# Kernel optimization log

Measured on AMD Instinct MI355X. Metric: run time of the kernel, lower is better.

The kernel has to match this reference:

```python
import jax, jax.numpy as jnp
import numpy as np

NUM_FRAMES = 64
H, W = 2048, 2048
MAX_DEPTH = 12


def setup_inputs() -> dict:
    key = jax.random.key(0)
    k1, k2, k3 = jax.random.split(key, 3)
    frame_colors = jax.random.uniform(k1, (NUM_FRAMES, 3), dtype=jnp.float32)
    frame_selection = jax.random.uniform(k2, (NUM_FRAMES, 2, NUM_FRAMES), dtype=jnp.float32)
    split_ratios = jax.random.uniform(k3, (NUM_FRAMES,), dtype=jnp.float32)
    return {
        "frame_colors": frame_colors,
        "frame_selection": frame_selection,
        "split_ratios": split_ratios,
    }


def reference(frame_colors, frame_selection, split_ratios):
    """Vectorized per-pixel descent of the bounded fractal recursion.

    Instead of recursive slice-assignments with host-synced argmax/.item(),
    each pixel tracks (frame idx, region origin, region size) and descends
    MAX_DEPTH levels via gathers. Equivalent math to render_frame(0,...).
    """
    # Per-frame child indices (argmax over the selection logits).
    left_child = jnp.argmax(frame_selection[:, 0, :], axis=-1).astype(jnp.int32)   # [F]
    right_child = jnp.argmax(frame_selection[:, 1, :], axis=-1).astype(jnp.int32)  # [F]

    yy, xx = jnp.meshgrid(jnp.arange(H, dtype=jnp.int32),
                          jnp.arange(W, dtype=jnp.int32), indexing="ij")  # [H,W]

    idx = jnp.zeros((H, W), jnp.int32)   # current frame index per pixel
    y0 = jnp.zeros((H, W), jnp.int32)    # region origin
    x0 = jnp.zeros((H, W), jnp.int32)
    h = jnp.full((H, W), H, jnp.int32)   # region size
    w = jnp.full((H, W), W, jnp.int32)
    done = jnp.zeros((H, W), bool)

    for _ in range(MAX_DEPTH):
        leaf = (w < 2) | (h < 2)            # base case: region too small
        act = (~done) & (~leaf)             # pixels that descend this level
        done = done | leaf

        ratio = split_ratios[idx]                       # [H,W]
        is_vert = (idx % 2) == 1                        # split_directions = i % 2
        # left_width = max(1, int(width * ratio)); analogous top_height
        lw = jnp.maximum(1, jnp.floor(w.astype(jnp.float32) * ratio).astype(jnp.int32))
        th = jnp.maximum(1, jnp.floor(h.astype(jnp.float32) * ratio).astype(jnp.int32))

        go_left = jnp.where(is_vert, (xx - x0) < lw, (yy - y0) < th)
        child = jnp.where(go_left, left_child[idx], right_child[idx])

        nx0 = jnp.where(is_vert & (~go_left), x0 + lw, x0)
        nw = jnp.where(is_vert, jnp.where(go_left, lw, w - lw), w)
        ny0 = jnp.where((~is_vert) & (~go_left), y0 + th, y0)
        nh = jnp.where(~is_vert, jnp.where(go_left, th, h - th), h)

        idx = jnp.where(act, child, idx)
        x0 = jnp.where(act, nx0, x0)
        w = jnp.where(act, nw, w)
        y0 = jnp.where(act, ny0, y0)
        h = jnp.where(act, nh, h)

    # Fill each pixel with its leaf frame's background color -> [3, H, W]
    out = frame_colors[idx]                 # [H, W, 3]
    return jnp.transpose(out, (2, 0, 1))
```

## Files before the change

### kernel.cpp

```cpp
#include <hip/hip_runtime.h>

#define HH_DIM 2048
#define WW_DIM 2048
#define NF 64
#define MAX_DEPTH 12

__global__ void child_argmax_kernel(const float* __restrict__ sel,
                                    int* __restrict__ child) {
    int r = threadIdx.x;
    if (r < 2 * NF) {
        const float* row = sel + r * NF;
        float best = row[0];
        int bi = 0;
        #pragma unroll
        for (int j = 1; j < NF; ++j) {
            float v = row[j];
            if (v > best) { best = v; bi = j; }
        }
        child[r] = bi;
    }
}

__global__ __launch_bounds__(256)
void render_kernel(const float* __restrict__ colors,
                   const float* __restrict__ ratios,
                   const int* __restrict__ child,
                   float* __restrict__ out) {
    __shared__ float s_ratio[NF];
    __shared__ int   s_child[2 * NF];
    __shared__ float s_col[3 * NF];

    int t = threadIdx.x;
    if (t < NF)      s_ratio[t] = ratios[t];
    if (t < 2 * NF)  s_child[t] = child[t];
    if (t < 3 * NF)  s_col[t]   = colors[t];
    __syncthreads();

    int gid = blockIdx.x * 256 + t;
    int y  = gid >> 9;
    int xb = (gid & 511) << 2;

    float c0[4], c1[4], c2[4];

    #pragma unroll
    for (int p = 0; p < 4; ++p) {
        int x = xb + p;
        int idx = 0;
        int x0 = 0, y0 = 0, w = WW_DIM, h = HH_DIM;
        for (int d = 0; d < MAX_DEPTH; ++d) {
            if (w < 2 || h < 2) break;
            float ratio = s_ratio[idx];
            int ni;
            if (idx & 1) {
                int lw = (int)floorf((float)w * ratio);
                lw = lw < 1 ? 1 : lw;
                bool left = (x - x0) < lw;
                ni = left ? s_child[2 * idx] : s_child[2 * idx + 1];
                if (left) { w = lw; }
                else      { x0 += lw; w -= lw; }
            } else {
                int th = (int)floorf((float)h * ratio);
                th = th < 1 ? 1 : th;
                bool left = (y - y0) < th;
                ni = left ? s_child[2 * idx] : s_child[2 * idx + 1];
                if (left) { h = th; }
                else      { y0 += th; h -= th; }
            }
            idx = ni;
        }
        c0[p] = s_col[idx * 3 + 0];
        c1[p] = s_col[idx * 3 + 1];
        c2[p] = s_col[idx * 3 + 2];
    }

    int base = y * WW_DIM + xb;
    const int plane = HH_DIM * WW_DIM;
    *(float4*)(out + base)             = make_float4(c0[0], c0[1], c0[2], c0[3]);
    *(float4*)(out + plane + base)     = make_float4(c1[0], c1[1], c1[2], c1[3]);
    *(float4*)(out + 2 * plane + base) = make_float4(c2[0], c2[1], c2[2], c2[3]);
}

extern "C" void kernel_launch(void* const* d_in, const int* in_sizes, int n_in,
                              void* d_out, int out_size, void* d_ws, size_t ws_size,
                              hipStream_t stream) {
    const float* frame_colors    = (const float*)d_in[0];
    const float* frame_selection = (const float*)d_in[1];
    const float* split_ratios    = (const float*)d_in[2];
    float* out = (float*)d_out;
    int* child = (int*)d_ws;

    child_argmax_kernel<<<1, 128, 0, stream>>>(frame_selection, child);

    render_kernel<<<4096, 256, 0, stream>>>(frame_colors, split_ratios, child, out);
}
```

Measured before the change: 96.69 us.

## Fuse argmax into render kernel and reuse descent across leaf-region pixel runs

The separate argmax launch is removed: every block recomputes the child indices from the selection logits in shared memory. Each thread now owns a 16-pixel strip of one row and runs the tree descent once per leaf region rather than once per pixel, filling every pixel up to the region's right edge. Leaf indices are packed as bytes into shared memory, then the block writes all three colour planes with coalesced float4 stores through a planar colour table. This cuts the per-pixel descent work and one launch, at the cost of redundant per-block argmax, an extra barrier and divergent while-loops across a wavefront.

Result: slower. 98.79 us (+2.2%).

```diff
diff --git a/kernel.cpp b/kernel.cpp
--- a/kernel.cpp
+++ b/kernel.cpp
@@ -1,83 +1,118 @@
 #include <hip/hip_runtime.h>
 
-#define HH_DIM 2048
-#define WW_DIM 2048
+#define HH 2048
+#define WW 2048
 #define NF 64
-#define MAX_DEPTH 12
+#define MAXD 12
+#define ROWS_PER_BLOCK 2
+#define STRIP 16
+#define PXB (ROWS_PER_BLOCK * WW)
 
-__global__ void child_argmax_kernel(const float* __restrict__ sel,
-                                    int* __restrict__ child) {
-    int r = threadIdx.x;
-    if (r < 2 * NF) {
-        const float* row = sel + r * NF;
-        float best = row[0];
+__global__ __launch_bounds__(256)
+void fractal_kernel(const float* __restrict__ colors,
+                    const float* __restrict__ sel,
+                    const float* __restrict__ ratios,
+                    float* __restrict__ out) {
+    __shared__ int2  s_node[NF];
+    __shared__ float s_colp[3 * NF];
+    __shared__ int   s_amax[2 * NF];
+    __shared__ unsigned char s_idx[PXB];
+
+    int t = threadIdx.x;
+
+    if (t < 2 * NF) {
+        const float4* row = (const float4*)(sel + t * NF);
+        float4 v0 = row[0];
+        float best = v0.x;
         int bi = 0;
         #pragma unroll
-        for (int j = 1; j < NF; ++j) {
-            float v = row[j];
-            if (v > best) { best = v; bi = j; }
+        for (int j = 0; j < NF / 4; ++j) {
+            float4 v = row[j];
+            if (v.x > best) { best = v.x; bi = 4 * j + 0; }
+            if (v.y > best) { best = v.y; bi = 4 * j + 1; }
+            if (v.z > best) { best = v.z; bi = 4 * j + 2; }
+            if (v.w > best) { best = v.w; bi = 4 * j + 3; }
         }
-        child[r] = bi;
+        s_amax[t] = bi;
     }
-}
-
-__global__ __launch_bounds__(256)
-void render_kernel(const float* __restrict__ colors,
-                   const float* __restrict__ ratios,
-                   const int* __restrict__ child,
-                   float* __restrict__ out) {
-    __shared__ float s_ratio[NF];
-    __shared__ int   s_child[2 * NF];
-    __shared__ float s_col[3 * NF];
-
-    int t = threadIdx.x;
-    if (t < NF)      s_ratio[t] = ratios[t];
-    if (t < 2 * NF)  s_child[t] = child[t];
-    if (t < 3 * NF)  s_col[t]   = colors[t];
+    if (t < NF) {
+        s_node[t].x = __float_as_int(ratios[t]);
+    }
+    if (t < 3 * NF) {
+        int f = t / 3, c = t - 3 * f;
+        s_colp[c * NF + f] = colors[t];
+    }
+    __syncthreads();
+    if (t < NF) {
+        s_node[t].y = s_amax[2 * t] | (s_amax[2 * t + 1] << 16);
+    }
     __syncthreads();
 
-    int gid = blockIdx.x * 256 + t;
-    int y  = gid >> 9;
-    int xb = (gid & 511) << 2;
+    int r  = t >> 7;
+    int c  = t & 127;
+    int y  = blockIdx.x * ROWS_PER_BLOCK + r;
+    int xb = c * STRIP;
+    int xend = xb + STRIP;
+    int x = xb;
+    unsigned long long lo = 0, hi = 0;
 
-    float c0[4], c1[4], c2[4];
-
-    #pragma unroll
-    for (int p = 0; p < 4; ++p) {
-        int x = xb + p;
-        int idx = 0;
-        int x0 = 0, y0 = 0, w = WW_DIM, h = HH_DIM;
-        for (int d = 0; d < MAX_DEPTH; ++d) {
-            if (w < 2 || h < 2) break;
-            float ratio = s_ratio[idx];
-            int ni;
-            if (idx & 1) {
-                int lw = (int)floorf((float)w * ratio);
-                lw = lw < 1 ? 1 : lw;
-                bool left = (x - x0) < lw;
-                ni = left ? s_child[2 * idx] : s_child[2 * idx + 1];
-                if (left) { w = lw; }
-                else      { x0 += lw; w -= lw; }
-            } else {
-                int th = (int)floorf((float)h * ratio);
-                th = th < 1 ? 1 : th;
-                bool left = (y - y0) < th;
-                ni = left ? s_child[2 * idx] : s_child[2 * idx + 1];
-                if (left) { h = th; }
-                else      { y0 += th; h -= th; }
+    while (__any(x < xend)) {
+        if (x < xend) {
+            int i = 0, x0 = 0, y0 = 0, w = WW, h = HH;
+            #pragma unroll 1
+            for (int d = 0; d < MAXD; ++d) {
+                if (w < 2 || h < 2) break;
+                int2 nd = s_node[i];
+                float ratio = __int_as_float(nd.x);
+                int chl = nd.y & 0xffff;
+                int chr = nd.y >> 16;
+                if (i & 1) {
+                    int lw = (int)floorf((float)w * ratio);
+                    lw = lw < 1 ? 1 : lw;
+                    if (x - x0 < lw) { i = chl; w = lw; }
+                    else             { i = chr; x0 += lw; w -= lw; }
+                } else {
+                    int th = (int)floorf((float)h * ratio);
+                    th = th < 1 ? 1 : th;
+                    if (y - y0 < th) { i = chl; h = th; }
+                    else             { i = chr; y0 += th; h -= th; }
+                }
             }
-            idx = ni;
+            int re = x0 + w;
+            if (re > xend) re = xend;
+            for (; x < re; ++x) {
+                int o = x - xb;
+                unsigned long long v =
+                    (unsigned long long)(unsigned)i << ((o & 7) * 8);
+                if (o < 8) lo |= v; else hi |= v;
+            }
         }
-        c0[p] = s_col[idx * 3 + 0];
-        c1[p] = s_col[idx * 3 + 1];
-        c2[p] = s_col[idx * 3 + 2];
     }
 
-    int base = y * WW_DIM + xb;
-    const int plane = HH_DIM * WW_DIM;
-    *(float4*)(out + base)             = make_float4(c0[0], c0[1], c0[2], c0[3]);
-    *(float4*)(out + plane + base)     = make_float4(c1[0], c1[1], c1[2], c1[3]);
-    *(float4*)(out + 2 * plane + base) = make_float4(c2[0], c2[1], c2[2], c2[3]);
+    {
+        ulonglong2 u;
+        u.x = lo; u.y = hi;
+        *(ulonglong2*)(s_idx + (r * WW + xb)) = u;
+    }
+    __syncthreads();
+
+    const int plane = HH * WW;
+    int base = blockIdx.x * PXB;
+    #pragma unroll
+    for (int pl = 0; pl < 3; ++pl) {
+        const float* cp = s_colp + pl * NF;
+        #pragma unroll
+        for (int j = 0; j < PXB / (256 * 4); ++j) {
+            int p4 = (j * 256 + t) * 4;
+            unsigned q = *(const unsigned*)(s_idx + p4);
+            float4 v;
+            v.x = cp[q & 0xff];
+            v.y = cp[(q >> 8) & 0xff];
+            v.z = cp[(q >> 16) & 0xff];
+            v.w = cp[q >> 24];
+            *(float4*)(out + pl * plane + base + p4) = v;
+        }
+    }
 }
 
 extern "C" void kernel_launch(void* const* d_in, const int* in_sizes, int n_in,
@@ -87,9 +122,7 @@
     const float* frame_selection = (const float*)d_in[1];
     const float* split_ratios    = (const float*)d_in[2];
     float* out = (float*)d_out;
-    int* child = (int*)d_ws;
 
-    child_argmax_kernel<<<1, 128, 0, stream>>>(frame_selection, child);
-
-    render_kernel<<<4096, 256, 0, stream>>>(frame_colors, split_ratios, child, out);
+    fractal_kernel<<<HH / ROWS_PER_BLOCK, 256, 0, stream>>>(
+        frame_colors, frame_selection, split_ratios, out);
 }
```
